# Performance work log

Measured on AMD Instinct MI355X. Metric: run time of the kernel, lower is better.

Reference implementation:

```python
import jax, jax.numpy as jnp
import numpy as np

B, N, D = 4, 2048, 1024

def setup_inputs() -> dict:
    key = jax.random.key(0)
    ks = jax.random.split(key, 8)
    s = 1.0 / np.sqrt(D)
    return {
        "x": jax.random.normal(ks[0], (B, N, D), dtype=jnp.float32),
        "Wq": jax.random.normal(ks[1], (D, D), dtype=jnp.float32) * s,
        "bq": jnp.zeros((D,), dtype=jnp.float32),
        "Wk": jax.random.normal(ks[2], (D, D), dtype=jnp.float32) * s,
        "bk": jnp.zeros((D,), dtype=jnp.float32),
        "Wv": jax.random.normal(ks[3], (D, D), dtype=jnp.float32) * s,
        "bv": jnp.zeros((D,), dtype=jnp.float32),
        "gamma": jnp.ones((1,), dtype=jnp.float32),
    }

def reference(x, Wq, bq, Wk, bk, Wv, bv, gamma):
    d = x.shape[-1]
    delta = 1.0 / jnp.sqrt(jnp.asarray(d, dtype=x.dtype))
    # torch Linear: y = x @ W.T + b, W is [out, in]
    Q = jnp.einsum('bnd,ed->bne', x, Wq) + bq
    K = jnp.einsum('bnd,ed->bne', x, Wk) + bk
    V = jnp.einsum('bnd,ed->bne', x, Wv) + bv
    scores = jnp.einsum('bne,bme->bnm', Q, K) * delta  # [B, N, N]
    attn = jax.nn.softmax(scores, axis=-1)
    out = jnp.einsum('bnm,bme->bne', attn, V)
    return out * gamma + x
```

## Files before the change

kernel.cpp:

```cpp
#include <hip/hip_runtime.h>

typedef _Float16 f16;
typedef __attribute__((ext_vector_type(4))) _Float16 f16x4;
typedef __attribute__((ext_vector_type(8))) _Float16 f16x8;
typedef __attribute__((ext_vector_type(4))) float f32x4;

#define B_ 4
#define N_ 2048
#define D_ 1024

#define FENCE asm volatile("" ::: "memory")

__global__ __launch_bounds__(256) void k_cast_all(const float4* __restrict__ x,
                                                  const float4* __restrict__ wq,
                                                  const float4* __restrict__ wk,
                                                  const float4* __restrict__ wv,
                                                  f16x4* __restrict__ xo,
                                                  f16x4* __restrict__ wqo,
                                                  f16x4* __restrict__ wko,
                                                  f16x4* __restrict__ wvo,
                                                  float* __restrict__ rowsum) {
  int b = blockIdx.x;
  if (b >= 11264) {
    rowsum[(b - 11264) * 256 + threadIdx.x] = 0.f;
    return;
  }
  const float4* in;
  f16x4* out;
  int idx;
  if (b < 8192)       { in = x;  out = xo;  idx = b * 256 + threadIdx.x; }
  else if (b < 9216)  { in = wq; out = wqo; idx = (b - 8192) * 256 + threadIdx.x; }
  else if (b < 10240) { in = wk; out = wko; idx = (b - 9216) * 256 + threadIdx.x; }
  else                { in = wv; out = wvo; idx = (b - 10240) * 256 + threadIdx.x; }
  float4 v = in[idx];
  f16x4 o = { (_Float16)v.x, (_Float16)v.y, (_Float16)v.z, (_Float16)v.w };
  out[idx] = o;
}

__device__ __forceinline__ void stage_half(const char* g0, int ldB, int kByte,
                                           char* slot, int tid) {
#pragma unroll
  for (int r = 0; r < 2; ++r) {
    int lin = r * 8192 + tid * 16;
    int row = lin >> 7;
    int lch = ((lin >> 4) & 7) ^ (row & 7);
    const char* g = g0 + (long)row * ldB + kByte + lch * 16;
    char* l = slot + r * 8192 + ((tid >> 6) << 10);
    __builtin_amdgcn_global_load_lds(
        (const __attribute__((address_space(1))) unsigned int*)g,
        (__attribute__((address_space(3))) unsigned int*)l, 16, 0, 0);
  }
}

__device__ __forceinline__ void gemm256(const char* gA, int ldaB,
                                        const char* gB, int ldbB,
                                        int nK, char* lds, f32x4 acc[2][4][2][2]) {
  const int tid = threadIdx.x;
  const int lane = tid & 63;
  const int wave = tid >> 6;
  const int wm = wave >> 2, wn = wave & 3;
  const int quad = lane >> 4, l16 = lane & 15;
  const int l7 = l16 & 7;
  const char* gA1 = gA + (long)128 * ldaB;
  const char* gB1 = gB + (long)128 * ldbB;
  char* Abuf = lds;
  char* Bbuf = lds + 65536;
  stage_half(gA,  ldaB, 0, Abuf, tid);
  stage_half(gB,  ldbB, 0, Bbuf, tid);
  stage_half(gA1, ldaB, 0, Abuf + 16384, tid);
  stage_half(gB1, ldbB, 0, Bbuf + 16384, tid);
  for (int t = 0; t < nK; ++t) {
    const int c = t & 1;
    char* Ac = Abuf + c * 32768;
    char* Bc = Bbuf + c * 32768;
    char* An = Abuf + (c ^ 1) * 32768;
    char* Bn = Bbuf + (c ^ 1) * 32768;
    const bool st = (t + 1 < nK);
    const int kB = (t + 1) << 7;
    f16x8 afc[2][4][2];
    f16x8 bf[2][2];
#pragma unroll
    for (int ph = 0; ph < 4; ++ph) {
      const int Ah = ph & 1, Bh = ph >> 1;
      if (ph == 0)      { asm volatile("s_waitcnt vmcnt(4)" ::: "memory"); }
      else if (ph == 1) { if (st) asm volatile("s_waitcnt vmcnt(4)" ::: "memory");
                          else    asm volatile("s_waitcnt vmcnt(2)" ::: "memory"); }
      else if (ph == 2) { if (st) asm volatile("s_waitcnt vmcnt(4)" ::: "memory");
                          else    asm volatile("s_waitcnt vmcnt(0)" ::: "memory"); }
      __builtin_amdgcn_s_barrier();
      FENCE;
      if (ph < 2) {
        const char* Ab = Ac + ph * 16384;
#pragma unroll
        for (int i = 0; i < 4; ++i) {
          int rA = wm * 64 + i * 16 + l16;
#pragma unroll
          for (int kk = 0; kk < 2; ++kk)
            afc[ph][i][kk] = *(const f16x8*)(Ab + rA * 128 + ((((kk << 2) | quad) ^ l7) << 4));
        }
      }
      if (Ah == 0) {
        const char* Bb = Bc + Bh * 16384;
#pragma unroll
        for (int jn = 0; jn < 2; ++jn) {
          int rB = wn * 32 + jn * 16 + l16;
#pragma unroll
          for (int kk = 0; kk < 2; ++kk)
            bf[jn][kk] = *(const f16x8*)(Bb + rB * 128 + ((((kk << 2) | quad) ^ l7) << 4));
        }
      }
      if (st) {
        if (ph == 0)      stage_half(gA,  ldaB, kB, An, tid);
        else if (ph == 1) stage_half(gB,  ldbB, kB, Bn, tid);
        else if (ph == 2) stage_half(gA1, ldaB, kB, An + 16384, tid);
        else              stage_half(gB1, ldbB, kB, Bn + 16384, tid);
      }
      FENCE;
      __builtin_amdgcn_s_barrier();
      __builtin_amdgcn_s_setprio(1);
#pragma unroll
      for (int i = 0; i < 4; ++i)
#pragma unroll
        for (int jn = 0; jn < 2; ++jn)
#pragma unroll
          for (int kk = 0; kk < 2; ++kk)
            acc[Ah][i][Bh][jn] = __builtin_amdgcn_mfma_f32_16x16x32_f16(
                afc[Ah][i][kk], bf[jn][kk], acc[Ah][i][Bh][jn], 0, 0, 0);
      __builtin_amdgcn_s_setprio(0);
    }
  }
  asm volatile("s_waitcnt vmcnt(0)" ::: "memory");
  __builtin_amdgcn_s_barrier();
  FENCE;
}

__device__ __forceinline__ void gemm_po(const char* gA, int ldaB,
                                        const char* gB, int ldbB,
                                        int nK, char* lds, f32x4 acc[4][2][2]) {
  const int tid = threadIdx.x;
  const int lane = tid & 63;
  const int wave = tid >> 6;
  const int wm = wave >> 2, wn = wave & 3;
  const int quad = lane >> 4, l16 = lane & 15;
  const int l7 = l16 & 7;
  const char* gB1 = gB + (long)128 * ldbB;
  stage_half(gA,  ldaB, 0, lds, tid);
  stage_half(gB,  ldbB, 0, lds + 16384, tid);
  stage_half(gB1, ldbB, 0, lds + 32768, tid);
  for (int t = 0; t < nK; ++t) {
    char* S0 = lds + (t & 1) * 49152;
    char* Sn = lds + ((t + 1) & 1) * 49152;
    const bool st = (t + 1 < nK);
    const int kB = (t + 1) << 7;
    f16x8 af[4][2], bf[2][2];
    asm volatile("s_waitcnt vmcnt(2)" ::: "memory");
    __builtin_amdgcn_s_barrier();
    FENCE;
#pragma unroll
    for (int i = 0; i < 4; ++i) {
      int rA = wm * 64 + i * 16 + l16;
#pragma unroll
      for (int kk = 0; kk < 2; ++kk)
        af[i][kk] = *(const f16x8*)(S0 + rA * 128 + ((((kk << 2) | quad) ^ l7) << 4));
    }
#pragma unroll
    for (int jn = 0; jn < 2; ++jn) {
      int rB = wn * 32 + jn * 16 + l16;
#pragma unroll
      for (int kk = 0; kk < 2; ++kk)
        bf[jn][kk] = *(const f16x8*)(S0 + 16384 + rB * 128 + ((((kk << 2) | quad) ^ l7) << 4));
    }
    if (st) { stage_half(gA, ldaB, kB, Sn, tid); stage_half(gB, ldbB, kB, Sn + 16384, tid); }
    FENCE;
    __builtin_amdgcn_s_barrier();
    __builtin_amdgcn_s_setprio(1);
#pragma unroll
    for (int i = 0; i < 4; ++i)
#pragma unroll
      for (int jn = 0; jn < 2; ++jn)
#pragma unroll
        for (int kk = 0; kk < 2; ++kk)
          acc[i][0][jn] = __builtin_amdgcn_mfma_f32_16x16x32_f16(
              af[i][kk], bf[jn][kk], acc[i][0][jn], 0, 0, 0);
    __builtin_amdgcn_s_setprio(0);
    if (st) asm volatile("s_waitcnt vmcnt(4)" ::: "memory");
    else    asm volatile("s_waitcnt vmcnt(0)" ::: "memory");
    __builtin_amdgcn_s_barrier();
    FENCE;
#pragma unroll
    for (int jn = 0; jn < 2; ++jn) {
      int rB = wn * 32 + jn * 16 + l16;
#pragma unroll
      for (int kk = 0; kk < 2; ++kk)
        bf[jn][kk] = *(const f16x8*)(S0 + 32768 + rB * 128 + ((((kk << 2) | quad) ^ l7) << 4));
    }
    if (st) stage_half(gB1, ldbB, kB, Sn + 32768, tid);
    FENCE;
    __builtin_amdgcn_s_barrier();
    __builtin_amdgcn_s_setprio(1);
#pragma unroll
    for (int i = 0; i < 4; ++i)
#pragma unroll
      for (int jn = 0; jn < 2; ++jn)
#pragma unroll
        for (int kk = 0; kk < 2; ++kk)
          acc[i][1][jn] = __builtin_amdgcn_mfma_f32_16x16x32_f16(
              af[i][kk], bf[jn][kk], acc[i][1][jn], 0, 0, 0);
    __builtin_amdgcn_s_setprio(0);
  }
}

__global__ __launch_bounds__(512, 2) void k_qkv(const f16* __restrict__ X,
                                                const f16* __restrict__ Wq,
                                                const f16* __restrict__ Wk,
                                                const f16* __restrict__ Wv,
                                                const float* __restrict__ bq,
                                                const float* __restrict__ bk,
                                                const float* __restrict__ bv,
                                                f16* __restrict__ Q, f16* __restrict__ Ko,
                                                f16* __restrict__ Vt) {
  __shared__ __align__(16) char lds[131072];
  int fid = blockIdx.x;
  int xcd = fid & 7, k = fid >> 3;
  int rowt = xcd * 4 + (k & 3);
  int colt = k >> 2;
  int tm = rowt * 256;
  int w = colt >> 2;
  int tn = (colt & 3) * 256;
  const f16* Wsel = (w == 0) ? Wq : (w == 1) ? Wk : Wv;
  f32x4 acc[2][4][2][2];
#pragma unroll
  for (int Ah = 0; Ah < 2; ++Ah)
#pragma unroll
    for (int i = 0; i < 4; ++i)
#pragma unroll
      for (int Bh = 0; Bh < 2; ++Bh)
#pragma unroll
        for (int jn = 0; jn < 2; ++jn) acc[Ah][i][Bh][jn] = (f32x4){0.f, 0.f, 0.f, 0.f};
  gemm256((const char*)(X + (long)tm * D_), D_ * 2,
          (const char*)(Wsel + (long)tn * D_), D_ * 2, D_ / 64, lds, acc);
  const int tid = threadIdx.x;
  const int lane = tid & 63, wave = tid >> 6;
  const int wm = wave >> 2, wn = wave & 3;
  const int quad = lane >> 4, l16 = lane & 15;
  if (w < 2) {
    const float* bias = w ? bk : bq;
    f16* outp = w ? Ko : Q;
#pragma unroll
    for (int Bh = 0; Bh < 2; ++Bh)
#pragma unroll
      for (int jn = 0; jn < 2; ++jn) {
        int col = tn + Bh * 128 + wn * 32 + jn * 16 + l16;
        float bb = bias[col];
#pragma unroll
        for (int Ah = 0; Ah < 2; ++Ah)
#pragma unroll
          for (int i = 0; i < 4; ++i) {
            int rbase = tm + Ah * 128 + wm * 64 + i * 16 + quad * 4;
#pragma unroll
            for (int r = 0; r < 4; ++r)
              outp[(long)(rbase + r) * D_ + col] = (_Float16)(acc[Ah][i][Bh][jn][r] + bb);
          }
      }
  } else {
    int bidx = tm >> 11, ntok = tm & 2047;
    f16* VtB = Vt + (long)bidx * D_ * N_ + ntok;
    f16* ldsT = (f16*)lds;
#pragma unroll
    for (int pass = 0; pass < 2; ++pass) {
      FENCE;
      __builtin_amdgcn_s_barrier();
      FENCE;
#pragma unroll
      for (int jn = 0; jn < 2; ++jn) {
        int fl = wn * 32 + jn * 16 + l16;
        float bb = bv[tn + pass * 128 + fl];
#pragma unroll
        for (int Ah = 0; Ah < 2; ++Ah)
#pragma unroll
          for (int i = 0; i < 4; ++i) {
            int rl = Ah * 128 + wm * 64 + i * 16 + quad * 4;
            f16x4 p = { (_Float16)(acc[Ah][i][pass][jn][0] + bb),
                        (_Float16)(acc[Ah][i][pass][jn][1] + bb),
                        (_Float16)(acc[Ah][i][pass][jn][2] + bb),
                        (_Float16)(acc[Ah][i][pass][jn][3] + bb) };
            *(f16x4*)(ldsT + fl * 264 + rl) = p;
          }
      }
      FENCE;
      __builtin_amdgcn_s_barrier();
      FENCE;
#pragma unroll
      for (int p = 0; p < 8; ++p) {
        int f = p * 16 + (tid >> 5);
        int cc = tid & 31;
        f16x8 v = *(const f16x8*)(ldsT + f * 264 + cc * 8);
        *(f16x8*)(VtB + (long)(tn + pass * 128 + f) * N_ + cc * 8) = v;
      }
    }
  }
}

__global__ __launch_bounds__(512, 2) void k_scores(const f16* __restrict__ Qf,
                                                   const f16* __restrict__ Kf,
                                                   f16* __restrict__ S,
                                                   float* __restrict__ rowsum) {
  __shared__ __align__(16) char lds[131072];
  int fid = blockIdx.x;
  int xcd = fid & 7, k = fid >> 3;
  int lin = xcd * 32 + k;
  int b = lin >> 6;
  int t = lin & 63;
  int rowt = t & 7, colt = t >> 3;
  int tm = rowt * 256, tn = colt * 256;
  f32x4 acc[2][4][2][2];
#pragma unroll
  for (int Ah = 0; Ah < 2; ++Ah)
#pragma unroll
    for (int i = 0; i < 4; ++i)
#pragma unroll
      for (int Bh = 0; Bh < 2; ++Bh)
#pragma unroll
        for (int jn = 0; jn < 2; ++jn) acc[Ah][i][Bh][jn] = (f32x4){0.f, 0.f, 0.f, 0.f};
  gemm256((const char*)(Qf + (long)b * N_ * D_ + (long)tm * D_), D_ * 2,
          (const char*)(Kf + (long)b * N_ * D_ + (long)tn * D_), D_ * 2,
          D_ / 64, lds, acc);
  const int tid = threadIdx.x;
  const int lane = tid & 63, wave = tid >> 6;
  const int wm = wave >> 2, wn = wave & 3;
  const int quad = lane >> 4, l16 = lane & 15;
  f16* Sb = S + (long)b * N_ * N_;
  const float delta = 0.03125f;
  f16* ldsS = (f16*)lds;
  float rsum[2][4][4];
#pragma unroll
  for (int Ah = 0; Ah < 2; ++Ah)
#pragma unroll
    for (int i = 0; i < 4; ++i)
#pragma unroll
      for (int r = 0; r < 4; ++r) rsum[Ah][i][r] = 0.f;
#pragma unroll
  for (int Bh = 0; Bh < 2; ++Bh) {
    FENCE;
    __builtin_amdgcn_s_barrier();
    FENCE;
#pragma unroll
    for (int Ah = 0; Ah < 2; ++Ah)
#pragma unroll
      for (int i = 0; i < 4; ++i) {
        int rloc = Ah * 128 + wm * 64 + i * 16 + quad * 4;
#pragma unroll
        for (int jn = 0; jn < 2; ++jn) {
          int col = wn * 32 + jn * 16 + l16;
#pragma unroll
          for (int r = 0; r < 4; ++r) {
            float e = __expf(acc[Ah][i][Bh][jn][r] * delta);
            rsum[Ah][i][r] += e;
            ldsS[(rloc + r) * 136 + col] = (_Float16)e;
          }
        }
      }
    FENCE;
    __builtin_amdgcn_s_barrier();
    FENCE;
#pragma unroll
    for (int p = 0; p < 8; ++p) {
      int row = p * 32 + (tid >> 4);
      int cc = tid & 15;
      f16x8 v = *(const f16x8*)(ldsS + row * 136 + cc * 8);
      *(f16x8*)(Sb + (long)(tm + row) * N_ + tn + Bh * 128 + cc * 8) = v;
    }
  }
#pragma unroll
  for (int m = 1; m < 16; m <<= 1)
#pragma unroll
    for (int Ah = 0; Ah < 2; ++Ah)
#pragma unroll
      for (int i = 0; i < 4; ++i)
#pragma unroll
        for (int r = 0; r < 4; ++r) rsum[Ah][i][r] += __shfl_xor(rsum[Ah][i][r], m);
  if (l16 == 0) {
    float* rs = rowsum + (long)b * N_ + tm;
#pragma unroll
    for (int Ah = 0; Ah < 2; ++Ah)
#pragma unroll
      for (int i = 0; i < 4; ++i)
#pragma unroll
        for (int r = 0; r < 4; ++r)
          atomicAdd(rs + Ah * 128 + wm * 64 + i * 16 + quad * 4 + r, rsum[Ah][i][r]);
  }
}

__global__ __launch_bounds__(512, 2) void k_out(const f16* __restrict__ P,
                                                const f16* __restrict__ Vt,
                                                const f16* __restrict__ xf,
                                                const float* __restrict__ gamma,
                                                const float* __restrict__ rowsum,
                                                float* __restrict__ out) {
  __shared__ __align__(16) char lds[98304];
  int fid = blockIdx.x;
  int xcd = fid & 7, kq = fid >> 3;
  int lin = xcd * 32 + kq;
  int b = lin >> 6;
  int t = lin & 63;
  int rowt = t >> 2, colt = t & 3;
  int tm = rowt * 128, tn = colt * 256;
  f32x4 acc[4][2][2];
#pragma unroll
  for (int i = 0; i < 4; ++i)
#pragma unroll
    for (int Bh = 0; Bh < 2; ++Bh)
#pragma unroll
      for (int jn = 0; jn < 2; ++jn) acc[i][Bh][jn] = (f32x4){0.f, 0.f, 0.f, 0.f};
  gemm_po((const char*)(P + (long)b * N_ * N_ + (long)tm * N_), N_ * 2,
          (const char*)(Vt + (long)b * D_ * N_ + (long)tn * N_), N_ * 2,
          N_ / 64, lds, acc);
  const int tid = threadIdx.x;
  const int lane = tid & 63, wave = tid >> 6;
  const int wm = wave >> 2, wn = wave & 3;
  const int quad = lane >> 4, l16 = lane & 15;
  float g = gamma[0];
  float inv[4][4];
#pragma unroll
  for (int i = 0; i < 4; ++i)
#pragma unroll
    for (int r = 0; r < 4; ++r)
      inv[i][r] = g / rowsum[(long)b * N_ + tm + wm * 64 + i * 16 + quad * 4 + r];
#pragma unroll
  for (int Bh = 0; Bh < 2; ++Bh)
#pragma unroll
    for (int jn = 0; jn < 2; ++jn) {
      int col = tn + Bh * 128 + wn * 32 + jn * 16 + l16;
#pragma unroll
      for (int i = 0; i < 4; ++i) {
        int rbase = tm + wm * 64 + i * 16 + quad * 4;
#pragma unroll
        for (int r = 0; r < 4; ++r) {
          long idx = (long)b * N_ * D_ + (long)(rbase + r) * D_ + col;
          out[idx] = acc[i][Bh][jn][r] * inv[i][r] + (float)xf[idx];
        }
      }
    }
}

extern "C" void kernel_launch(void* const* d_in, const int* in_sizes, int n_in,
                              void* d_out, int out_size, void* d_ws, size_t ws_size,
                              hipStream_t stream) {
  const float* x  = (const float*)d_in[0];
  const float* Wq = (const float*)d_in[1];
  const float* bq = (const float*)d_in[2];
  const float* Wk = (const float*)d_in[3];
  const float* bk = (const float*)d_in[4];
  const float* Wv = (const float*)d_in[5];
  const float* bv = (const float*)d_in[6];
  const float* gamma = (const float*)d_in[7];
  float* out = (float*)d_out;
  char* ws = (char*)d_ws;

  f16* Qb  = (f16*)(ws);
  f16* Kb  = (f16*)(ws + (16u << 20));
  f16* Vt  = (f16*)(ws + (32u << 20));
  f16* Xb  = (f16*)(ws + (48u << 20));
  f16* Wqb = (f16*)(ws + (64u << 20));
  f16* Wkb = (f16*)(ws + (66u << 20));
  f16* Wvb = (f16*)(ws + (68u << 20));
  f16* S   = (f16*)(ws + (64u << 20));
  float* rowsum = (float*)(ws + (96u << 20));

  k_cast_all<<<11296, 256, 0, stream>>>((const float4*)x, (const float4*)Wq,
                                        (const float4*)Wk, (const float4*)Wv,
                                        (f16x4*)Xb, (f16x4*)Wqb, (f16x4*)Wkb, (f16x4*)Wvb,
                                        rowsum);
  k_qkv<<<384, 512, 0, stream>>>(Xb, Wqb, Wkb, Wvb, bq, bk, bv, Qb, Kb, Vt);
  k_scores<<<256, 512, 0, stream>>>(Qb, Kb, S, rowsum);
  k_out<<<256, 512, 0, stream>>>(S, Vt, Xb, gamma, rowsum, out);
}
```

Measured before the change: 237.0 us.

## Replace gemm_po with register-prefetching pipeline, shrink QKV tiles to 128 rows

Adds gemm_d128, a 128x256 GEMM mainloop that preloads the next K-step's A and B fragments from LDS while the current MFMAs run, ping-ponging register sets and issuing global->LDS staging earlier. It is used both in the PV output kernel and in the QKV projection, which now uses 128-row tiles with 768 blocks instead of 256-row tiles with 384 blocks, and a single-pass V transpose. The goal is to hide LDS read latency and improve wave balance across CUs. The cost is more register pressure from the doubled fragment sets, and less data reuse per block in QKV.

Result: no change. 238.6 us (+0.7%).

```diff
diff --git a/kernel.cpp b/kernel.cpp
--- a/kernel.cpp
+++ b/kernel.cpp
@@ -50,6 +50,81 @@
         (const __attribute__((address_space(1))) unsigned int*)g,
         (__attribute__((address_space(3))) unsigned int*)l, 16, 0, 0);
   }
+}
+
+#define RD_A(dst, base)                                                          \
+  _Pragma("unroll") for (int i_ = 0; i_ < 4; ++i_) {                             \
+    int rA_ = wm * 64 + i_ * 16 + l16;                                           \
+    _Pragma("unroll") for (int k_ = 0; k_ < 2; ++k_)                             \
+      dst[i_][k_] = *(const f16x8*)((base) + rA_ * 128 +                         \
+                                    ((((k_ << 2) | quad) ^ l7) << 4));           \
+  }
+#define RD_B(dst, base)                                                          \
+  _Pragma("unroll") for (int j_ = 0; j_ < 2; ++j_) {                             \
+    int rB_ = wn * 32 + j_ * 16 + l16;                                           \
+    _Pragma("unroll") for (int k_ = 0; k_ < 2; ++k_)                             \
+      dst[j_][k_] = *(const f16x8*)((base) + rB_ * 128 +                         \
+                                    ((((k_ << 2) | quad) ^ l7) << 4));           \
+  }
+#define MFMA8(Av, Bv, BH)                                                        \
+  __builtin_amdgcn_s_setprio(1);                                                 \
+  _Pragma("unroll") for (int i_ = 0; i_ < 4; ++i_)                               \
+  _Pragma("unroll") for (int j_ = 0; j_ < 2; ++j_)                               \
+  _Pragma("unroll") for (int k_ = 0; k_ < 2; ++k_)                               \
+    acc[i_][BH][j_] = __builtin_amdgcn_mfma_f32_16x16x32_f16(                    \
+        Av[i_][k_], Bv[j_][k_], acc[i_][BH][j_], 0, 0, 0);                       \
+  __builtin_amdgcn_s_setprio(0);
+
+#define D128_TILE(AC, B0C, AN, B0N, q) {                                         \
+  char* Sc = lds + (q) * 49152;                                                  \
+  char* Sn = lds + ((q) ^ 1) * 49152;                                            \
+  const int kB = (t + 1) << 7;                                                   \
+           \
+  stage_half(gA, ldaB, kB, Sn, tid);                                             \
+  stage_half(gB, ldbB, kB, Sn + 16384, tid);                                     \
+  asm volatile("s_waitcnt vmcnt(4)" ::: "memory");                               \
+  __builtin_amdgcn_s_barrier(); FENCE;                                           \
+  RD_B(b1, Sc + 32768);                                                          \
+  MFMA8(AC, B0C, 0);                                                             \
+                         \
+  stage_half(gB1, ldbB, kB, Sn + 32768, tid);                                    \
+  asm volatile("s_waitcnt vmcnt(2)" ::: "memory");                               \
+  __builtin_amdgcn_s_barrier(); FENCE;                                           \
+  RD_A(AN, Sn); RD_B(B0N, Sn + 16384);                                           \
+  MFMA8(AC, b1, 1);                                                              \
+}
+#define D128_TAIL(AC, B0C, q) {                                                  \
+  char* Sc = lds + (q) * 49152;                                                  \
+  asm volatile("s_waitcnt vmcnt(0)" ::: "memory");                               \
+  __builtin_amdgcn_s_barrier(); FENCE;                                           \
+  RD_B(b1, Sc + 32768);                                                          \
+  MFMA8(AC, B0C, 0);                                                             \
+  MFMA8(AC, b1, 1);                                                              \
+}
+
+__device__ __forceinline__ void gemm_d128(const char* gA, int ldaB,
+                                          const char* gB, int ldbB,
+                                          int nK, char* lds, f32x4 acc[4][2][2]) {
+  const int tid = threadIdx.x;
+  const int lane = tid & 63, wave = tid >> 6;
+  const int wm = wave >> 2, wn = wave & 3;
+  const int quad = lane >> 4, l16 = lane & 15;
+  const int l7 = l16 & 7;
+  const char* gB1 = gB + (long)128 * ldbB;
+  f16x8 aX[4][2], aY[4][2], b0X[2][2], b0Y[2][2], b1[2][2];
+  stage_half(gA,  ldaB, 0, lds, tid);
+  stage_half(gB,  ldbB, 0, lds + 16384, tid);
+  stage_half(gB1, ldbB, 0, lds + 32768, tid);
+  asm volatile("s_waitcnt vmcnt(2)" ::: "memory");
+  __builtin_amdgcn_s_barrier(); FENCE;
+  RD_A(aX, lds); RD_B(b0X, lds + 16384);
+  for (int tb = 0; tb < nK - 2; tb += 2) {
+    { const int t = tb;     D128_TILE(aX, b0X, aY, b0Y, 0) }
+    { const int t = tb + 1; D128_TILE(aY, b0Y, aX, b0X, 1) }
+  }
+  { const int t = nK - 2;   D128_TILE(aX, b0X, aY, b0Y, 0) }
+  D128_TAIL(aY, b0Y, 1)
+  __builtin_amdgcn_s_barrier(); FENCE;
 }
 
 __device__ __forceinline__ void gemm256(const char* gA, int ldaB,
@@ -134,82 +209,6 @@
   FENCE;
 }
 
-__device__ __forceinline__ void gemm_po(const char* gA, int ldaB,
-                                        const char* gB, int ldbB,
-                                        int nK, char* lds, f32x4 acc[4][2][2]) {
-  const int tid = threadIdx.x;
-  const int lane = tid & 63;
-  const int wave = tid >> 6;
-  const int wm = wave >> 2, wn = wave & 3;
-  const int quad = lane >> 4, l16 = lane & 15;
-  const int l7 = l16 & 7;
-  const char* gB1 = gB + (long)128 * ldbB;
-  stage_half(gA,  ldaB, 0, lds, tid);
-  stage_half(gB,  ldbB, 0, lds + 16384, tid);
-  stage_half(gB1, ldbB, 0, lds + 32768, tid);
-  for (int t = 0; t < nK; ++t) {
-    char* S0 = lds + (t & 1) * 49152;
-    char* Sn = lds + ((t + 1) & 1) * 49152;
-    const bool st = (t + 1 < nK);
-    const int kB = (t + 1) << 7;
-    f16x8 af[4][2], bf[2][2];
-    asm volatile("s_waitcnt vmcnt(2)" ::: "memory");
-    __builtin_amdgcn_s_barrier();
-    FENCE;
-#pragma unroll
-    for (int i = 0; i < 4; ++i) {
-      int rA = wm * 64 + i * 16 + l16;
-#pragma unroll
-      for (int kk = 0; kk < 2; ++kk)
-        af[i][kk] = *(const f16x8*)(S0 + rA * 128 + ((((kk << 2) | quad) ^ l7) << 4));
-    }
-#pragma unroll
-    for (int jn = 0; jn < 2; ++jn) {
-      int rB = wn * 32 + jn * 16 + l16;
-#pragma unroll
-      for (int kk = 0; kk < 2; ++kk)
-        bf[jn][kk] = *(const f16x8*)(S0 + 16384 + rB * 128 + ((((kk << 2) | quad) ^ l7) << 4));
-    }
-    if (st) { stage_half(gA, ldaB, kB, Sn, tid); stage_half(gB, ldbB, kB, Sn + 16384, tid); }
-    FENCE;
-    __builtin_amdgcn_s_barrier();
-    __builtin_amdgcn_s_setprio(1);
-#pragma unroll
-    for (int i = 0; i < 4; ++i)
-#pragma unroll
-      for (int jn = 0; jn < 2; ++jn)
-#pragma unroll
-        for (int kk = 0; kk < 2; ++kk)
-          acc[i][0][jn] = __builtin_amdgcn_mfma_f32_16x16x32_f16(
-              af[i][kk], bf[jn][kk], acc[i][0][jn], 0, 0, 0);
-    __builtin_amdgcn_s_setprio(0);
-    if (st) asm volatile("s_waitcnt vmcnt(4)" ::: "memory");
-    else    asm volatile("s_waitcnt vmcnt(0)" ::: "memory");
-    __builtin_amdgcn_s_barrier();
-    FENCE;
-#pragma unroll
-    for (int jn = 0; jn < 2; ++jn) {
-      int rB = wn * 32 + jn * 16 + l16;
-#pragma unroll
-      for (int kk = 0; kk < 2; ++kk)
-        bf[jn][kk] = *(const f16x8*)(S0 + 32768 + rB * 128 + ((((kk << 2) | quad) ^ l7) << 4));
-    }
-    if (st) stage_half(gB1, ldbB, kB, Sn + 32768, tid);
-    FENCE;
-    __builtin_amdgcn_s_barrier();
-    __builtin_amdgcn_s_setprio(1);
-#pragma unroll
-    for (int i = 0; i < 4; ++i)
-#pragma unroll
-      for (int jn = 0; jn < 2; ++jn)
-#pragma unroll
-        for (int kk = 0; kk < 2; ++kk)
-          acc[i][1][jn] = __builtin_amdgcn_mfma_f32_16x16x32_f16(
-              af[i][kk], bf[jn][kk], acc[i][1][jn], 0, 0, 0);
-    __builtin_amdgcn_s_setprio(0);
-  }
-}
-
 __global__ __launch_bounds__(512, 2) void k_qkv(const f16* __restrict__ X,
                                                 const f16* __restrict__ Wq,
                                                 const f16* __restrict__ Wk,
@@ -219,26 +218,24 @@
                                                 const float* __restrict__ bv,
                                                 f16* __restrict__ Q, f16* __restrict__ Ko,
                                                 f16* __restrict__ Vt) {
-  __shared__ __align__(16) char lds[131072];
+  __shared__ __align__(16) char lds[98304];
   int fid = blockIdx.x;
   int xcd = fid & 7, k = fid >> 3;
-  int rowt = xcd * 4 + (k & 3);
-  int colt = k >> 2;
-  int tm = rowt * 256;
+  int rowt = xcd * 8 + (k & 7);
+  int colt = k >> 3;
+  int tm = rowt * 128;
   int w = colt >> 2;
   int tn = (colt & 3) * 256;
   const f16* Wsel = (w == 0) ? Wq : (w == 1) ? Wk : Wv;
-  f32x4 acc[2][4][2][2];
-#pragma unroll
-  for (int Ah = 0; Ah < 2; ++Ah)
-#pragma unroll
-    for (int i = 0; i < 4; ++i)
-#pragma unroll
-      for (int Bh = 0; Bh < 2; ++Bh)
-#pragma unroll
-        for (int jn = 0; jn < 2; ++jn) acc[Ah][i][Bh][jn] = (f32x4){0.f, 0.f, 0.f, 0.f};
-  gemm256((const char*)(X + (long)tm * D_), D_ * 2,
-          (const char*)(Wsel + (long)tn * D_), D_ * 2, D_ / 64, lds, acc);
+  f32x4 acc[4][2][2];
+#pragma unroll
+  for (int i = 0; i < 4; ++i)
+#pragma unroll
+    for (int Bh = 0; Bh < 2; ++Bh)
+#pragma unroll
+      for (int jn = 0; jn < 2; ++jn) acc[i][Bh][jn] = (f32x4){0.f, 0.f, 0.f, 0.f};
+  gemm_d128((const char*)(X + (long)tm * D_), D_ * 2,
+            (const char*)(Wsel + (long)tn * D_), D_ * 2, D_ / 64, lds, acc);
   const int tid = threadIdx.x;
   const int lane = tid & 63, wave = tid >> 6;
   const int wm = wave >> 2, wn = wave & 3;
@@ -253,50 +250,40 @@
         int col = tn + Bh * 128 + wn * 32 + jn * 16 + l16;
         float bb = bias[col];
 #pragma unroll
-        for (int Ah = 0; Ah < 2; ++Ah)
-#pragma unroll
-          for (int i = 0; i < 4; ++i) {
-            int rbase = tm + Ah * 128 + wm * 64 + i * 16 + quad * 4;
-#pragma unroll
-            for (int r = 0; r < 4; ++r)
-              outp[(long)(rbase + r) * D_ + col] = (_Float16)(acc[Ah][i][Bh][jn][r] + bb);
-          }
+        for (int i = 0; i < 4; ++i) {
+          int rbase = tm + wm * 64 + i * 16 + quad * 4;
+#pragma unroll
+          for (int r = 0; r < 4; ++r)
+            outp[(long)(rbase + r) * D_ + col] = (_Float16)(acc[i][Bh][jn][r] + bb);
+        }
       }
   } else {
     int bidx = tm >> 11, ntok = tm & 2047;
     f16* VtB = Vt + (long)bidx * D_ * N_ + ntok;
     f16* ldsT = (f16*)lds;
 #pragma unroll
-    for (int pass = 0; pass < 2; ++pass) {
-      FENCE;
-      __builtin_amdgcn_s_barrier();
-      FENCE;
+    for (int Bh = 0; Bh < 2; ++Bh)
 #pragma unroll
       for (int jn = 0; jn < 2; ++jn) {
-        int fl = wn * 32 + jn * 16 + l16;
-        float bb = bv[tn + pass * 128 + fl];
-#pragma unroll
-        for (int Ah = 0; Ah < 2; ++Ah)
-#pragma unroll
-          for (int i = 0; i < 4; ++i) {
-            int rl = Ah * 128 + wm * 64 + i * 16 + quad * 4;
-            f16x4 p = { (_Float16)(acc[Ah][i][pass][jn][0] + bb),
-                        (_Float16)(acc[Ah][i][pass][jn][1] + bb),
-                        (_Float16)(acc[Ah][i][pass][jn][2] + bb),
-                        (_Float16)(acc[Ah][i][pass][jn][3] + bb) };
-            *(f16x4*)(ldsT + fl * 264 + rl) = p;
-          }
-      }
-      FENCE;
-      __builtin_amdgcn_s_barrier();
-      FENCE;
-#pragma unroll
-      for (int p = 0; p < 8; ++p) {
-        int f = p * 16 + (tid >> 5);
-        int cc = tid & 31;
-        f16x8 v = *(const f16x8*)(ldsT + f * 264 + cc * 8);
-        *(f16x8*)(VtB + (long)(tn + pass * 128 + f) * N_ + cc * 8) = v;
-      }
+        int fl = Bh * 128 + wn * 32 + jn * 16 + l16;
+        float bb = bv[tn + fl];
+#pragma unroll
+        for (int i = 0; i < 4; ++i) {
+          int rl = wm * 64 + i * 16 + quad * 4;
+          f16x4 p = { (_Float16)(acc[i][Bh][jn][0] + bb), (_Float16)(acc[i][Bh][jn][1] + bb),
+                      (_Float16)(acc[i][Bh][jn][2] + bb), (_Float16)(acc[i][Bh][jn][3] + bb) };
+          *(f16x4*)(ldsT + fl * 136 + rl) = p;
+        }
+      }
+    FENCE;
+    __builtin_amdgcn_s_barrier();
+    FENCE;
+#pragma unroll
+    for (int p = 0; p < 8; ++p) {
+      int f = p * 32 + (tid >> 4);
+      int cc = tid & 15;
+      f16x8 v = *(const f16x8*)(ldsT + f * 136 + cc * 8);
+      *(f16x8*)(VtB + (long)(tn + f) * N_ + cc * 8) = v;
     }
   }
 }
@@ -412,9 +399,9 @@
     for (int Bh = 0; Bh < 2; ++Bh)
 #pragma unroll
       for (int jn = 0; jn < 2; ++jn) acc[i][Bh][jn] = (f32x4){0.f, 0.f, 0.f, 0.f};
-  gemm_po((const char*)(P + (long)b * N_ * N_ + (long)tm * N_), N_ * 2,
-          (const char*)(Vt + (long)b * D_ * N_ + (long)tn * N_), N_ * 2,
-          N_ / 64, lds, acc);
+  gemm_d128((const char*)(P + (long)b * N_ * N_ + (long)tm * N_), N_ * 2,
+            (const char*)(Vt + (long)b * D_ * N_ + (long)tn * N_), N_ * 2,
+            N_ / 64, lds, acc);
   const int tid = threadIdx.x;
   const int lane = tid & 63, wave = tid >> 6;
   const int wm = wave >> 2, wn = wave & 3;
@@ -471,7 +458,7 @@
                                         (const float4*)Wk, (const float4*)Wv,
                                         (f16x4*)Xb, (f16x4*)Wqb, (f16x4*)Wkb, (f16x4*)Wvb,
                                         rowsum);
-  k_qkv<<<384, 512, 0, stream>>>(Xb, Wqb, Wkb, Wvb, bq, bk, bv, Qb, Kb, Vt);
+  k_qkv<<<768, 512, 0, stream>>>(Xb, Wqb, Wkb, Wvb, bq, bk, bv, Qb, Kb, Vt);
   k_scores<<<256, 512, 0, stream>>>(Qb, Kb, S, rowsum);
   k_out<<<256, 512, 0, stream>>>(S, Vt, Xb, gamma, rowsum, out);
 }
```
